# Kernel tuning notes

Hardware: AMD Instinct MI355X
Metric: run time of the kernel (lower is better)

## Reference

```python
import jax, jax.numpy as jnp
import numpy as np


def setup_inputs() -> dict:
    key = jax.random.key(0)
    ks = jax.random.split(key, 10)
    B, T, C, E, H, W = 32, 768, 448, 256, 56, 56
    s = 0.02  # param init scale
    return {
        "text_feature": jax.random.normal(ks[0], (B, T), jnp.float32),
        "image_feature": jax.random.normal(ks[1], (B, C, H, W), jnp.float32),
        "q_w": jax.random.normal(ks[2], (E, T), jnp.float32) * s,
        "q_b": jax.random.normal(ks[3], (E,), jnp.float32) * s,
        "k_w": jax.random.normal(ks[4], (E, C), jnp.float32) * s,
        "k_b": jax.random.normal(ks[5], (E,), jnp.float32) * s,
        "v_w": jax.random.normal(ks[6], (E, C), jnp.float32) * s,
        "v_b": jax.random.normal(ks[7], (E,), jnp.float32) * s,
        "o_w": jax.random.normal(ks[8], (C, E), jnp.float32) * s,
        "o_b": jax.random.normal(ks[9], (C,), jnp.float32) * s,
    }


def reference(text_feature, image_feature, q_w, q_b, k_w, k_b, v_w, v_b, o_w, o_b):
    B, C, H, W = image_feature.shape
    E = q_w.shape[0]
    # query: Linear(text_dim -> embed_dim)  -> [B, E]
    q = text_feature @ q_w.T + q_b
    # key/value: 1x1 conv == per-pixel linear over channels -> [B, E, H*W]
    img = image_feature.reshape(B, C, H * W)          # [B, C, N]
    k = jnp.einsum("ec,bcn->ben", k_w, img) + k_b[None, :, None]
    v = jnp.einsum("ec,bcn->ben", v_w, img) + v_b[None, :, None]
    # single-query attention over spatial positions
    scale = 1.0 / jnp.sqrt(jnp.asarray(E, image_feature.dtype))
    attn = jax.nn.softmax(jnp.einsum("be,ben->bn", q, k) * scale, axis=-1)  # [B, N]
    pooled = jnp.einsum("bn,ben->be", attn, v)        # [B, E]
    # output 1x1 conv on a spatially-constant map == linear once, then broadcast
    out = pooled @ o_w.T + o_b                        # [B, C]
    return image_feature + out[:, :, None, None]
```

## Files before the change

### kernel.cpp

```cpp
#include <hip/hip_runtime.h>
#include <math.h>

#define B_  32
#define T_  768
#define C_  448
#define E_  256
#define N_  3136
#define N4_ 784
#define CCHUNK_ 16
#define CPER_   28
#define TOTAL4_ 11239424

__global__ __launch_bounds__(256) void k1_qk(
    const float* __restrict__ text, const float* __restrict__ q_w,
    const float* __restrict__ q_b,  const float* __restrict__ k_w,
    float* __restrict__ qk)
{
    const int b = blockIdx.x, tid = threadIdx.x;
    __shared__ float t_lds[T_];
    __shared__ float q_lds[E_];
    for (int i = tid; i < T_; i += 256) t_lds[i] = text[b * T_ + i];
    __syncthreads();
    {
        const int e = tid;
        float acc = q_b[e];
        const float* qw = q_w + (size_t)e * T_;
        #pragma unroll 4
        for (int t = 0; t < T_; ++t) acc = fmaf(t_lds[t], qw[t], acc);
        q_lds[e] = acc;
    }
    __syncthreads();
    const float scale = 0.0625f;
    for (int c = tid; c < C_; c += 256) {
        float acc = 0.f;
        for (int e = 0; e < E_; ++e) acc = fmaf(q_lds[e], k_w[e * C_ + c], acc);
        qk[b * C_ + c] = acc * scale;
    }
}

__global__ __launch_bounds__(256) void k2_logits(
    const float* __restrict__ img, const float* __restrict__ qk,
    float* __restrict__ partial)
{
    const int cy = blockIdx.x;
    const int b  = blockIdx.y;
    const int tid = threadIdx.x;
    const int c0 = cy * CPER_;

    __shared__ float w_lds[CPER_];
    if (tid < CPER_) w_lds[tid] = qk[b * C_ + c0 + tid];
    __syncthreads();

    float4 a0 = {0.f,0.f,0.f,0.f}, a1 = {0.f,0.f,0.f,0.f};
    float4 a2 = {0.f,0.f,0.f,0.f}, a3 = {0.f,0.f,0.f,0.f};
    const float4* imgb = (const float4*)img + (size_t)(b * C_ + c0) * N4_;
    const bool tail = (tid < (N4_ - 768));

    for (int c = 0; c < CPER_; ++c) {
        const float w = w_lds[c];
        const float4* row = imgb + (size_t)c * N4_;
        float4 x0 = row[tid];
        float4 x1 = row[tid + 256];
        float4 x2 = row[tid + 512];
        a0.x = fmaf(w, x0.x, a0.x); a0.y = fmaf(w, x0.y, a0.y);
        a0.z = fmaf(w, x0.z, a0.z); a0.w = fmaf(w, x0.w, a0.w);
        a1.x = fmaf(w, x1.x, a1.x); a1.y = fmaf(w, x1.y, a1.y);
        a1.z = fmaf(w, x1.z, a1.z); a1.w = fmaf(w, x1.w, a1.w);
        a2.x = fmaf(w, x2.x, a2.x); a2.y = fmaf(w, x2.y, a2.y);
        a2.z = fmaf(w, x2.z, a2.z); a2.w = fmaf(w, x2.w, a2.w);
        if (tail) {
            float4 x3 = row[tid + 768];
            a3.x = fmaf(w, x3.x, a3.x); a3.y = fmaf(w, x3.y, a3.y);
            a3.z = fmaf(w, x3.z, a3.z); a3.w = fmaf(w, x3.w, a3.w);
        }
    }
    float4* p = (float4*)partial + (size_t)(cy * B_ + b) * N4_;
    p[tid]       = a0;
    p[tid + 256] = a1;
    p[tid + 512] = a2;
    if (tail) p[tid + 768] = a3;
}

__global__ __launch_bounds__(256) void k3_softmax(
    const float* __restrict__ partial, float* __restrict__ attn)
{
    const int b = blockIdx.x, tid = threadIdx.x;
    __shared__ float4 l4[N4_];
    __shared__ float redm[4];
    __shared__ float reds[4];

    float lmax = -1e30f;
    for (int i4 = tid; i4 < N4_; i4 += 256) {
        float4 s = {0.f,0.f,0.f,0.f};
        for (int cy = 0; cy < CCHUNK_; ++cy) {
            const float4 p = ((const float4*)partial)[(size_t)(cy * B_ + b) * N4_ + i4];
            s.x += p.x; s.y += p.y; s.z += p.z; s.w += p.w;
        }
        l4[i4] = s;
        lmax = fmaxf(lmax, fmaxf(fmaxf(s.x, s.y), fmaxf(s.z, s.w)));
    }
    for (int off = 32; off; off >>= 1) lmax = fmaxf(lmax, __shfl_down(lmax, off));
    if ((tid & 63) == 0) redm[tid >> 6] = lmax;
    __syncthreads();
    const float m = fmaxf(fmaxf(redm[0], redm[1]), fmaxf(redm[2], redm[3]));

    float lsum = 0.f;
    for (int i4 = tid; i4 < N4_; i4 += 256) {
        float4 v = l4[i4];
        v.x = expf(v.x - m); v.y = expf(v.y - m);
        v.z = expf(v.z - m); v.w = expf(v.w - m);
        l4[i4] = v;
        lsum += v.x + v.y + v.z + v.w;
    }
    for (int off = 32; off; off >>= 1) lsum += __shfl_down(lsum, off);
    if ((tid & 63) == 0) reds[tid >> 6] = lsum;
    __syncthreads();
    const float inv = 1.f / (reds[0] + reds[1] + reds[2] + reds[3]);

    for (int i4 = tid; i4 < N4_; i4 += 256) {
        float4 v = l4[i4];
        v.x *= inv; v.y *= inv; v.z *= inv; v.w *= inv;
        ((float4*)attn)[(size_t)b * N4_ + i4] = v;
    }
}

__global__ __launch_bounds__(64) void k4_pool(
    const float* __restrict__ img, const float* __restrict__ attn,
    float* __restrict__ pimg)
{
    const int c = blockIdx.x, b = blockIdx.y, tid = threadIdx.x;
    const float4* row = (const float4*)img + (size_t)(b * C_ + c) * N4_;
    const float4* at  = (const float4*)attn + (size_t)b * N4_;
    float4 acc = {0.f,0.f,0.f,0.f};
    for (int i4 = tid; i4 < N4_; i4 += 64) {
        const float4 x = row[i4];
        const float4 a = at[i4];
        acc.x = fmaf(a.x, x.x, acc.x); acc.y = fmaf(a.y, x.y, acc.y);
        acc.z = fmaf(a.z, x.z, acc.z); acc.w = fmaf(a.w, x.w, acc.w);
    }
    float s = acc.x + acc.y + acc.z + acc.w;
    for (int off = 32; off; off >>= 1) s += __shfl_down(s, off);
    if (tid == 0) pimg[b * C_ + c] = s;
}

__global__ __launch_bounds__(256) void k5_out(
    const float* __restrict__ pimg, const float* __restrict__ v_w,
    const float* __restrict__ v_b,  const float* __restrict__ o_w,
    const float* __restrict__ o_b,  float* __restrict__ outvec)
{
    const int b = blockIdx.x, tid = threadIdx.x;
    __shared__ float p_lds[C_];
    __shared__ float e_lds[E_];
    for (int c = tid; c < C_; c += 256) p_lds[c] = pimg[b * C_ + c];
    __syncthreads();
    {
        const int e = tid;
        float acc = v_b[e];
        const float* vw = v_w + (size_t)e * C_;
        for (int c = 0; c < C_; ++c) acc = fmaf(vw[c], p_lds[c], acc);
        e_lds[e] = acc;
    }
    __syncthreads();
    for (int c = tid; c < C_; c += 256) {
        float acc = o_b[c];
        const float* ow = o_w + (size_t)c * E_;
        for (int e = 0; e < E_; ++e) acc = fmaf(ow[e], e_lds[e], acc);
        outvec[b * C_ + c] = acc;
    }
}

__global__ __launch_bounds__(256) void k6_add(
    const float* __restrict__ img, const float* __restrict__ outvec,
    float* __restrict__ out)
{
    const unsigned i = blockIdx.x * 256u + threadIdx.x;
    const float4 x = ((const float4*)img)[i];
    const float o = outvec[i / N4_];
    float4 r;
    r.x = x.x + o; r.y = x.y + o; r.z = x.z + o; r.w = x.w + o;
    ((float4*)out)[i] = r;
}

extern "C" void kernel_launch(void* const* d_in, const int* in_sizes, int n_in,
                              void* d_out, int out_size, void* d_ws, size_t ws_size,
                              hipStream_t stream) {
    const float* text = (const float*)d_in[0];
    const float* img  = (const float*)d_in[1];
    const float* q_w  = (const float*)d_in[2];
    const float* q_b  = (const float*)d_in[3];
    const float* k_w  = (const float*)d_in[4];
    const float* k_b  = (const float*)d_in[5];
    const float* v_w  = (const float*)d_in[6];
    const float* v_b  = (const float*)d_in[7];
    const float* o_w  = (const float*)d_in[8];
    const float* o_b  = (const float*)d_in[9];
    float* out = (float*)d_out;
    (void)k_b; (void)in_sizes; (void)n_in; (void)out_size; (void)ws_size;

    float* ws      = (float*)d_ws;
    float* qk      = ws;
    float* partial = qk + B_ * C_;
    float* attn    = partial + CCHUNK_ * B_ * N_;
    float* pimg    = attn + B_ * N_;
    float* outvec  = pimg + B_ * C_;

    k1_qk<<<B_, 256, 0, stream>>>(text, q_w, q_b, k_w, qk);
    k2_logits<<<dim3(CCHUNK_, B_), 256, 0, stream>>>(img, qk, partial);
    k3_softmax<<<B_, 256, 0, stream>>>(partial, attn);
    k4_pool<<<dim3(C_, B_), 64, 0, stream>>>(img, attn, pimg);
    k5_out<<<B_, 256, 0, stream>>>(pimg, v_w, v_b, o_w, o_b, outvec);
    k6_add<<<TOTAL4_ / 256, 256, 0, stream>>>(img, outvec, out);
}
```

Measured before the change: 503.4 us.

## Fuse logits, softmax and pooling into spatial-tiled kernel with split-softmax combine

Replaces the separate logits, softmax and pooling kernels with a single kernel that tiles the spatial dimension into 16 tiles per batch. Each block computes local logits, a local max and exp-sum, and locally weighted pooled channel sums, so the image tile is re-read while it is likely still in cache. A combine kernel then rescales the per-tile partials flash-attention style before the value and output projections. This removes the large partial-logit buffer and one full pass over the image, but only 49 of 64 lanes per wave are active and the per-channel shuffle reductions add overhead. Unroll pragmas are also added to the small GEMV loops.

```diff
diff --git a/kernel.cpp b/kernel.cpp
--- a/kernel.cpp
+++ b/kernel.cpp
@@ -7,11 +7,11 @@
 #define E_  256
 #define N_  3136
 #define N4_ 784
-#define CCHUNK_ 16
-#define CPER_   28
+#define NTILE_ 16
+#define NT4_ 49
 #define TOTAL4_ 11239424
 
-__global__ __launch_bounds__(256) void k1_qk(
+__global__ __launch_bounds__(256) void kA_qk(
     const float* __restrict__ text, const float* __restrict__ q_w,
     const float* __restrict__ q_b,  const float* __restrict__ k_w,
     float* __restrict__ qk)
@@ -25,7 +25,7 @@
         const int e = tid;
         float acc = q_b[e];
         const float* qw = q_w + (size_t)e * T_;
-        #pragma unroll 4
+        #pragma unroll 8
         for (int t = 0; t < T_; ++t) acc = fmaf(t_lds[t], qw[t], acc);
         q_lds[e] = acc;
     }
@@ -33,130 +33,126 @@
     const float scale = 0.0625f;
     for (int c = tid; c < C_; c += 256) {
         float acc = 0.f;
+        #pragma unroll 4
         for (int e = 0; e < E_; ++e) acc = fmaf(q_lds[e], k_w[e * C_ + c], acc);
         qk[b * C_ + c] = acc * scale;
     }
 }
 
-__global__ __launch_bounds__(256) void k2_logits(
+__global__ __launch_bounds__(256) void kB_logits_pool(
     const float* __restrict__ img, const float* __restrict__ qk,
-    float* __restrict__ partial)
-{
-    const int cy = blockIdx.x;
-    const int b  = blockIdx.y;
+    float* __restrict__ Ppart,
+    float* __restrict__ msloc)
+{
+    const int t = blockIdx.x;
+    const int b = blockIdx.y;
     const int tid = threadIdx.x;
-    const int c0 = cy * CPER_;
-
-    __shared__ float w_lds[CPER_];
-    if (tid < CPER_) w_lds[tid] = qk[b * C_ + c0 + tid];
-    __syncthreads();
-
-    float4 a0 = {0.f,0.f,0.f,0.f}, a1 = {0.f,0.f,0.f,0.f};
-    float4 a2 = {0.f,0.f,0.f,0.f}, a3 = {0.f,0.f,0.f,0.f};
-    const float4* imgb = (const float4*)img + (size_t)(b * C_ + c0) * N4_;
-    const bool tail = (tid < (N4_ - 768));
-
-    for (int c = 0; c < CPER_; ++c) {
-        const float w = w_lds[c];
-        const float4* row = imgb + (size_t)c * N4_;
-        float4 x0 = row[tid];
-        float4 x1 = row[tid + 256];
-        float4 x2 = row[tid + 512];
-        a0.x = fmaf(w, x0.x, a0.x); a0.y = fmaf(w, x0.y, a0.y);
-        a0.z = fmaf(w, x0.z, a0.z); a0.w = fmaf(w, x0.w, a0.w);
-        a1.x = fmaf(w, x1.x, a1.x); a1.y = fmaf(w, x1.y, a1.y);
-        a1.z = fmaf(w, x1.z, a1.z); a1.w = fmaf(w, x1.w, a1.w);
-        a2.x = fmaf(w, x2.x, a2.x); a2.y = fmaf(w, x2.y, a2.y);
-        a2.z = fmaf(w, x2.z, a2.z); a2.w = fmaf(w, x2.w, a2.w);
-        if (tail) {
-            float4 x3 = row[tid + 768];
-            a3.x = fmaf(w, x3.x, a3.x); a3.y = fmaf(w, x3.y, a3.y);
-            a3.z = fmaf(w, x3.z, a3.z); a3.w = fmaf(w, x3.w, a3.w);
-        }
-    }
-    float4* p = (float4*)partial + (size_t)(cy * B_ + b) * N4_;
-    p[tid]       = a0;
-    p[tid + 256] = a1;
-    p[tid + 512] = a2;
-    if (tail) p[tid + 768] = a3;
-}
-
-__global__ __launch_bounds__(256) void k3_softmax(
-    const float* __restrict__ partial, float* __restrict__ attn)
-{
-    const int b = blockIdx.x, tid = threadIdx.x;
-    __shared__ float4 l4[N4_];
-    __shared__ float redm[4];
-    __shared__ float reds[4];
-
-    float lmax = -1e30f;
-    for (int i4 = tid; i4 < N4_; i4 += 256) {
-        float4 s = {0.f,0.f,0.f,0.f};
-        for (int cy = 0; cy < CCHUNK_; ++cy) {
-            const float4 p = ((const float4*)partial)[(size_t)(cy * B_ + b) * N4_ + i4];
-            s.x += p.x; s.y += p.y; s.z += p.z; s.w += p.w;
-        }
-        l4[i4] = s;
-        lmax = fmaxf(lmax, fmaxf(fmaxf(s.x, s.y), fmaxf(s.z, s.w)));
-    }
-    for (int off = 32; off; off >>= 1) lmax = fmaxf(lmax, __shfl_down(lmax, off));
-    if ((tid & 63) == 0) redm[tid >> 6] = lmax;
-    __syncthreads();
-    const float m = fmaxf(fmaxf(redm[0], redm[1]), fmaxf(redm[2], redm[3]));
-
-    float lsum = 0.f;
-    for (int i4 = tid; i4 < N4_; i4 += 256) {
-        float4 v = l4[i4];
-        v.x = expf(v.x - m); v.y = expf(v.y - m);
-        v.z = expf(v.z - m); v.w = expf(v.w - m);
-        l4[i4] = v;
-        lsum += v.x + v.y + v.z + v.w;
-    }
-    for (int off = 32; off; off >>= 1) lsum += __shfl_down(lsum, off);
-    if ((tid & 63) == 0) reds[tid >> 6] = lsum;
-    __syncthreads();
-    const float inv = 1.f / (reds[0] + reds[1] + reds[2] + reds[3]);
-
-    for (int i4 = tid; i4 < N4_; i4 += 256) {
-        float4 v = l4[i4];
-        v.x *= inv; v.y *= inv; v.z *= inv; v.w *= inv;
-        ((float4*)attn)[(size_t)b * N4_ + i4] = v;
-    }
-}
-
-__global__ __launch_bounds__(64) void k4_pool(
-    const float* __restrict__ img, const float* __restrict__ attn,
-    float* __restrict__ pimg)
-{
-    const int c = blockIdx.x, b = blockIdx.y, tid = threadIdx.x;
-    const float4* row = (const float4*)img + (size_t)(b * C_ + c) * N4_;
-    const float4* at  = (const float4*)attn + (size_t)b * N4_;
-    float4 acc = {0.f,0.f,0.f,0.f};
-    for (int i4 = tid; i4 < N4_; i4 += 64) {
-        const float4 x = row[i4];
-        const float4 a = at[i4];
-        acc.x = fmaf(a.x, x.x, acc.x); acc.y = fmaf(a.y, x.y, acc.y);
-        acc.z = fmaf(a.z, x.z, acc.z); acc.w = fmaf(a.w, x.w, acc.w);
-    }
-    float s = acc.x + acc.y + acc.z + acc.w;
-    for (int off = 32; off; off >>= 1) s += __shfl_down(s, off);
-    if (tid == 0) pimg[b * C_ + c] = s;
-}
-
-__global__ __launch_bounds__(256) void k5_out(
-    const float* __restrict__ pimg, const float* __restrict__ v_w,
-    const float* __restrict__ v_b,  const float* __restrict__ o_w,
-    const float* __restrict__ o_b,  float* __restrict__ outvec)
+    const int w = tid >> 6, lane = tid & 63;
+
+    __shared__ float  qk_lds[C_];
+    __shared__ float4 plog[4][NT4_];
+    __shared__ float4 w_lds[NT4_];
+
+    for (int c = tid; c < C_; c += 256) qk_lds[c] = qk[b * C_ + c];
+    __syncthreads();
+
+    const float4* imgb = (const float4*)img + (size_t)(b * C_) * N4_ + t * NT4_;
+
+    const int c0 = w * 112;
+    if (lane < NT4_) {
+        float4 acc = {0.f, 0.f, 0.f, 0.f};
+        #pragma unroll 4
+        for (int k = 0; k < 112; ++k) {
+            const float qkc = qk_lds[c0 + k];
+            const float4 x = imgb[(size_t)(c0 + k) * N4_ + lane];
+            acc.x = fmaf(qkc, x.x, acc.x); acc.y = fmaf(qkc, x.y, acc.y);
+            acc.z = fmaf(qkc, x.z, acc.z); acc.w = fmaf(qkc, x.w, acc.w);
+        }
+        plog[w][lane] = acc;
+    }
+    __syncthreads();
+
+    if (w == 0) {
+        float4 l4;
+        float m = -1e30f;
+        if (lane < NT4_) {
+            l4 = plog[0][lane];
+            const float4 p1 = plog[1][lane], p2 = plog[2][lane], p3 = plog[3][lane];
+            l4.x += p1.x + p2.x + p3.x; l4.y += p1.y + p2.y + p3.y;
+            l4.z += p1.z + p2.z + p3.z; l4.w += p1.w + p2.w + p3.w;
+            m = fmaxf(fmaxf(l4.x, l4.y), fmaxf(l4.z, l4.w));
+        }
+        for (int off = 32; off; off >>= 1) m = fmaxf(m, __shfl_xor(m, off));
+        float s = 0.f;
+        if (lane < NT4_) {
+            float4 e4;
+            e4.x = expf(l4.x - m); e4.y = expf(l4.y - m);
+            e4.z = expf(l4.z - m); e4.w = expf(l4.w - m);
+            w_lds[lane] = e4;
+            s = e4.x + e4.y + e4.z + e4.w;
+        }
+        for (int off = 32; off; off >>= 1) s += __shfl_xor(s, off);
+        if (lane == 0) {
+            msloc[(b * NTILE_ + t) * 2 + 0] = m;
+            msloc[(b * NTILE_ + t) * 2 + 1] = s;
+        }
+    }
+    __syncthreads();
+
+    #pragma unroll 2
+    for (int k = 0; k < 112; ++k) {
+        const int c = c0 + k;
+        float p = 0.f;
+        if (lane < NT4_) {
+            const float4 x  = imgb[(size_t)c * N4_ + lane];
+            const float4 ww = w_lds[lane];
+            p = ww.x * x.x + ww.y * x.y + ww.z * x.z + ww.w * x.w;
+        }
+        for (int off = 32; off; off >>= 1) p += __shfl_xor(p, off);
+        if (lane == 0) Ppart[((size_t)b * NTILE_ + t) * C_ + c] = p;
+    }
+}
+
+__global__ __launch_bounds__(256) void kC_combine(
+    const float* __restrict__ Ppart, const float* __restrict__ msloc,
+    const float* __restrict__ v_w,   const float* __restrict__ v_b,
+    const float* __restrict__ o_w,   const float* __restrict__ o_b,
+    float* __restrict__ outvec)
 {
     const int b = blockIdx.x, tid = threadIdx.x;
     __shared__ float p_lds[C_];
     __shared__ float e_lds[E_];
-    for (int c = tid; c < C_; c += 256) p_lds[c] = pimg[b * C_ + c];
+    __shared__ float scl[NTILE_];
+    __shared__ float invD_sh;
+
+    if (tid == 0) {
+        float M = -1e30f;
+        for (int t = 0; t < NTILE_; ++t)
+            M = fmaxf(M, msloc[(b * NTILE_ + t) * 2]);
+        float D = 0.f;
+        for (int t = 0; t < NTILE_; ++t) {
+            const float e = expf(msloc[(b * NTILE_ + t) * 2] - M);
+            scl[t] = e;
+            D = fmaf(msloc[(b * NTILE_ + t) * 2 + 1], e, D);
+        }
+        invD_sh = 1.f / D;
+    }
+    __syncthreads();
+    const float invD = invD_sh;
+
+    for (int c = tid; c < C_; c += 256) {
+        float s = 0.f;
+        #pragma unroll
+        for (int t = 0; t < NTILE_; ++t)
+            s = fmaf(Ppart[((size_t)b * NTILE_ + t) * C_ + c], scl[t], s);
+        p_lds[c] = s * invD;
+    }
     __syncthreads();
     {
         const int e = tid;
         float acc = v_b[e];
         const float* vw = v_w + (size_t)e * C_;
+        #pragma unroll 4
         for (int c = 0; c < C_; ++c) acc = fmaf(vw[c], p_lds[c], acc);
         e_lds[e] = acc;
     }
@@ -164,12 +160,13 @@
     for (int c = tid; c < C_; c += 256) {
         float acc = o_b[c];
         const float* ow = o_w + (size_t)c * E_;
+        #pragma unroll 4
         for (int e = 0; e < E_; ++e) acc = fmaf(ow[e], e_lds[e], acc);
         outvec[b * C_ + c] = acc;
     }
 }
 
-__global__ __launch_bounds__(256) void k6_add(
+__global__ __launch_bounds__(256) void kD_add(
     const float* __restrict__ img, const float* __restrict__ outvec,
     float* __restrict__ out)
 {
@@ -197,17 +194,14 @@
     float* out = (float*)d_out;
     (void)k_b; (void)in_sizes; (void)n_in; (void)out_size; (void)ws_size;
 
-    float* ws      = (float*)d_ws;
-    float* qk      = ws;
-    float* partial = qk + B_ * C_;
-    float* attn    = partial + CCHUNK_ * B_ * N_;
-    float* pimg    = attn + B_ * N_;
-    float* outvec  = pimg + B_ * C_;
-
-    k1_qk<<<B_, 256, 0, stream>>>(text, q_w, q_b, k_w, qk);
-    k2_logits<<<dim3(CCHUNK_, B_), 256, 0, stream>>>(img, qk, partial);
-    k3_softmax<<<B_, 256, 0, stream>>>(partial, attn);
-    k4_pool<<<dim3(C_, B_), 64, 0, stream>>>(img, attn, pimg);
-    k5_out<<<B_, 256, 0, stream>>>(pimg, v_w, v_b, o_w, o_b, outvec);
-    k6_add<<<TOTAL4_ / 256, 256, 0, stream>>>(img, outvec, out);
-}
+    float* ws     = (float*)d_ws;
+    float* qk     = ws;
+    float* Ppart  = qk + B_ * C_;
+    float* msloc  = Ppart + B_ * NTILE_ * C_;
+    float* outvec = msloc + B_ * NTILE_ * 2;
+
+    kA_qk<<<B_, 256, 0, stream>>>(text, q_w, q_b, k_w, qk);
+    kB_logits_pool<<<dim3(NTILE_, B_), 256, 0, stream>>>(img, qk, Ppart, msloc);
+    kC_combine<<<B_, 256, 0, stream>>>(Ppart, msloc, v_w, v_b, o_w, o_b, outvec);
+    kD_add<<<TOTAL4_ / 256, 256, 0, stream>>>(img, outvec, out);
+}
```

After: 534.2 us. +6.1%, slower.
